# Kernel optimization log

Hardware: AMD Instinct MI355X
Metric: run time of the kernel (lower is better)

Reference implementation:

```python
import jax, jax.numpy as jnp
import numpy as np
from jax import lax

B, N, C, W, D = 128, 16384, 8, 10, 3   # batch, input_size, n_channels, out_window, poly_degree
L = N - W + 1                          # in-filter tap length
EPS = 1e-5


def setup_inputs() -> dict:
    key = jax.random.key(0)
    ks = jax.random.split(key, 8)
    x = jax.random.normal(ks[0], (B, N, C, 2), dtype=jnp.float32)
    # torch Linear-style scale ~ 1/sqrt(fan_in)
    w_in_real = jax.random.normal(ks[1], (C, L), dtype=jnp.float32) * (L ** -0.5)
    w_in_imag = jax.random.normal(ks[2], (C, L), dtype=jnp.float32) * (L ** -0.5)
    fan_coeff = 2 * (C - 1) * D
    w_coeff = jax.random.normal(ks[3], (C, 2, fan_coeff), dtype=jnp.float32) * (fan_coeff ** -0.5)
    w_out_real = jax.random.normal(ks[4], (C, W), dtype=jnp.float32) * (W ** -0.5)
    w_out_imag = jax.random.normal(ks[5], (C, W), dtype=jnp.float32) * (W ** -0.5)
    bn_gamma = jnp.ones((C,), dtype=jnp.float32)
    bn_beta = jnp.zeros((C,), dtype=jnp.float32)
    return {"x": x, "w_in_real": w_in_real, "w_in_imag": w_in_imag,
            "w_coeff": w_coeff, "w_out_real": w_out_real,
            "w_out_imag": w_out_imag, "bn_gamma": bn_gamma, "bn_beta": bn_beta}


# complement index map: row c lists all channels != c
_IDX = np.array([[j for j in range(C) if j != c] for c in range(C)])  # (C, C-1)


def _grouped_fir(sig, w):
    # sig: (B, N, C); per-channel length-L correlation -> (B, W, C)
    out = lax.conv_general_dilated(
        jnp.transpose(sig, (0, 2, 1)),      # (B, C, N)
        w[:, None, :],                      # (C, 1, L)
        window_strides=(1,), padding='VALID', feature_group_count=C)
    return jnp.transpose(out, (0, 2, 1))    # (B, W, C)


def reference(x, w_in_real, w_in_imag, w_coeff, w_out_real, w_out_imag, bn_gamma, bn_beta):
    fr = _grouped_fir(x[..., 0], w_in_real)   # (B, W, C)
    fi = _grouped_fir(x[..., 1], w_in_imag)   # (B, W, C)

    # polynomial expansion: pow_d = fr^d + fi^d, d = 1..D
    powd = jnp.stack([fr ** d + fi ** d for d in range(1, D + 1)], axis=-1)  # (B, W, C, D)
    poly_r = powd * fr[..., None]
    poly_i = powd * fi[..., None]

    # cross-channel coeff layers: input layout = [real(all j != c), imag(all j != c)]
    rg = poly_r[:, :, _IDX, :]                      # (B, W, C, C-1, D)
    ig = poly_i[:, :, _IDX, :]
    Wc = w_coeff.reshape(C, 2, 2, C - 1, D)         # (c, out, real/imag half, j, d)
    nonlin = (jnp.einsum('bwcjd,cpjd->bwcp', rg, Wc[:, :, 0]) +
              jnp.einsum('bwcjd,cpjd->bwcp', ig, Wc[:, :, 1]))  # (B, W, C, 2)

    out_r = jnp.einsum('bwc,cw->bc', nonlin[..., 0], w_out_real)
    out_i = jnp.einsum('bwc,cw->bc', nonlin[..., 1], w_out_imag)
    out = jnp.stack([out_r, out_i], axis=-1)        # (B, C, 2)

    # BatchNorm1d over (batch, last) per channel, training-mode batch stats
    mean = out.mean(axis=(0, 2), keepdims=True)
    var = out.var(axis=(0, 2), keepdims=True)
    return (out - mean) / jnp.sqrt(var + EPS) * bn_gamma[None, :, None] + bn_beta[None, :, None]
```

## Files before the change

kernel.cpp:

```cpp
#include <hip/hip_runtime.h>

#define BB 128
#define NN 16384
#define CC 8
#define WW 10
#define LL 16375
#define NT 512
#define NTILES (NN / NT)
#define BT 8
#define BTILES (BB / BT)
#define WSL (NT + 9)
#define SWSZ (WSL * 4 + 17)
#define BPB 2
#define ABLK (BB / BPB)

typedef float f4_t __attribute__((ext_vector_type(4)));

__global__ __launch_bounds__(512, 2) void k_fir(const float* __restrict__ x,
                                                const float* __restrict__ wr,
                                                const float* __restrict__ wi,
                                                float* __restrict__ fpart2) {
  __shared__ f4_t sw[SWSZ];
  int nt = blockIdx.x & (NTILES - 1);
  int bt = blockIdx.x >> 5;
  int tid = threadIdx.x;
  int ntile = nt * NT;
  int l0 = ntile - 9;

  {
    int c2s = tid & 3;
    int ca = 2 * c2s, cb = ca + 1;
    for (int j = tid >> 2; j < WSL; j += 128) {
      int l = l0 + j;
      f4_t v = (f4_t)0.f;
      if (l >= 0 && l < LL) {
        v[0] = wr[(size_t)ca * LL + l];
        v[1] = wi[(size_t)ca * LL + l];
        v[2] = wr[(size_t)cb * LL + l];
        v[3] = wi[(size_t)cb * LL + l];
      }
      sw[j * 4 + c2s + (j >> 5)] = v;
    }
  }
  __syncthreads();

  int wvb = tid >> 6;
  int b   = bt * BT + wvb;
  int c2  = tid & 3;
  int s   = (tid >> 2) & 15;
  int jbase = s * 32 + 9;

  const f4_t* __restrict__ xp = (const f4_t*)x + ((size_t)b * NN + ntile + s * 32) * 4 + c2;

#define TAP(q) sw[(jbase + (q)) * 4 + c2 + ((jbase + (q)) >> 5)]

  f4_t acc[WW];
#pragma unroll
  for (int w = 0; w < WW; ++w) acc[w] = (f4_t)0.f;

  f4_t wv[16];
#pragma unroll
  for (int k = 0; k < 9; ++k) wv[7 + k] = TAP(k - 9);

#pragma unroll
  for (int g = 0; g < 2; ++g) {
#pragma unroll
    for (int j = 0; j < 7; ++j) wv[j] = TAP(16 * g + j);
#pragma unroll
    for (int u = 0; u < 16; ++u) {
      f4_t xv = xp[(size_t)(16 * g + u) * 4];
#pragma unroll
      for (int w = 0; w < WW; ++w) {
        f4_t wt = wv[(u - w + 16) & 15];
        acc[w] += xv * wt;
      }
      if (u <= 8) wv[u + 7] = TAP(16 * g + u + 7);
    }
  }

#pragma unroll
  for (int w = 0; w < WW; ++w)
#pragma unroll
    for (int e = 0; e < 4; ++e) {
      acc[w][e] += __shfl_xor(acc[w][e], 4);
      acc[w][e] += __shfl_xor(acc[w][e], 8);
      acc[w][e] += __shfl_xor(acc[w][e], 16);
      acc[w][e] += __shfl_xor(acc[w][e], 32);
    }

  int lane = tid & 63;
  if (lane < 40) {
    int wsel = lane >> 2;
    f4_t myacc = (f4_t)0.f;
#pragma unroll
    for (int w = 0; w < WW; ++w)
      if (w == wsel) myacc = acc[w];
#pragma unroll
    for (int e = 0; e < 4; ++e)
      fpart2[((size_t)(wsel * 16 + c2 * 4 + e) * BB + b) * NTILES + nt] = myacc[e];
  }
}

__global__ __launch_bounds__(256) void k_nonlin(const float* __restrict__ fpart2,
                                                const float* __restrict__ wc,
                                                const float* __restrict__ wor,
                                                const float* __restrict__ woi,
                                                float* __restrict__ oraw,
                                                float* __restrict__ part) {
  __shared__ float sred[BPB][164];
  __shared__ float swc[672];
  __shared__ float swout[160];

  int tid = threadIdx.x;
  int blk = blockIdx.x;
  int b0 = blk * BPB;

  for (int i = tid; i < 672; i += 256) swc[i] = wc[i];
  if (tid < 80) swout[tid] = wor[tid];
  else if (tid < 160) swout[tid] = woi[tid - 80];

  for (int t = tid; t < 2 * 160; t += 256) {
    int r = t >> 1, bl = t & 1;
    const f4_t* fp = (const f4_t*)(fpart2 + ((size_t)r * BB + b0 + bl) * NTILES);
    f4_t s4 = (f4_t)0.f;
#pragma unroll
    for (int k = 0; k < NTILES / 4; ++k) s4 += fp[k];
    sred[bl][r] = s4[0] + s4[1] + s4[2] + s4[3];
  }
  __syncthreads();

  if (tid < 32) {
    int bl = tid >> 4;
    int c  = (tid >> 1) & 7;
    int p  = tid & 1;

    float wreg[8][2][3];
#pragma unroll
    for (int j = 0; j < 8; ++j) {
      int jj = j - (j > c ? 1 : 0);
      if (j == c) jj = 0;
#pragma unroll
      for (int ri = 0; ri < 2; ++ri)
#pragma unroll
        for (int d = 0; d < 3; ++d) {
          float v = swc[(c * 2 + p) * 42 + ri * 21 + jj * 3 + d];
          wreg[j][ri][d] = (j == c) ? 0.f : v;
        }
    }

    float o = 0.f;
    const float* wop = swout + p * 80 + c * 10;
#pragma unroll
    for (int w = 0; w < WW; ++w) {
      float4 f0 = *(const float4*)&sred[bl][w * 16];
      float4 f1 = *(const float4*)&sred[bl][w * 16 + 4];
      float4 f2 = *(const float4*)&sred[bl][w * 16 + 8];
      float4 f3 = *(const float4*)&sred[bl][w * 16 + 12];
      float fv[16] = {f0.x, f0.y, f0.z, f0.w, f1.x, f1.y, f1.z, f1.w,
                      f2.x, f2.y, f2.z, f2.w, f3.x, f3.y, f3.z, f3.w};
      float nl0 = 0.f, nl1 = 0.f, nl2 = 0.f;
#pragma unroll
      for (int j = 0; j < 8; ++j) {
        float r  = fv[2 * j];
        float im = fv[2 * j + 1];
        float r2 = r * r, i2 = im * im;
        float pw0 = r + im;
        float pw1 = r2 + i2;
        float pw2 = r2 * r + i2 * im;
        nl0 += (pw0 * r) * wreg[j][0][0] + (pw0 * im) * wreg[j][1][0];
        nl1 += (pw1 * r) * wreg[j][0][1] + (pw1 * im) * wreg[j][1][1];
        nl2 += (pw2 * r) * wreg[j][0][2] + (pw2 * im) * wreg[j][1][2];
      }
      o += (nl0 + nl1 + nl2) * wop[w];
    }

    oraw[((size_t)(b0 + bl) * CC + c) * 2 + p] = o;

    float s = o, q = o * o;
    s += __shfl_xor(s, 1);  q += __shfl_xor(q, 1);
    s += __shfl_xor(s, 16); q += __shfl_xor(q, 16);
    if ((tid & 17) == 0) {
      part[blk * 16 + c * 2 + 0] = s;
      part[blk * 16 + c * 2 + 1] = q;
    }
  }
}

__global__ __launch_bounds__(256) void k_bn(const float* __restrict__ oraw,
                                            const float* __restrict__ part,
                                            const float* __restrict__ gamma,
                                            const float* __restrict__ beta,
                                            float* __restrict__ out) {
  __shared__ float mv[8], iv[8], bv[8];
  int tid = threadIdx.x;
  if (tid < 16) {
    int cc = tid >> 1, qq = tid & 1;
    float s = 0.f;
#pragma unroll
    for (int k = 0; k < ABLK; ++k) s += part[k * 16 + cc * 2 + qq];
    float other = __shfl_xor(s, 1);
    if (qq == 0) {
      float mean = s * (1.0f / 256.0f);
      float var  = other * (1.0f / 256.0f) - mean * mean;
      mv[cc] = mean;
      iv[cc] = gamma[cc] * rsqrtf(var + 1e-5f);
      bv[cc] = beta[cc];
    }
  }
  __syncthreads();
  for (int i = tid; i < BB * CC * 2; i += 256) {
    int c = (i >> 1) & 7;
    out[i] = (oraw[i] - mv[c]) * iv[c] + bv[c];
  }
}

extern "C" void kernel_launch(void* const* d_in, const int* in_sizes, int n_in,
                              void* d_out, int out_size, void* d_ws, size_t ws_size,
                              hipStream_t stream) {
  const float* x   = (const float*)d_in[0];
  const float* wr  = (const float*)d_in[1];
  const float* wi  = (const float*)d_in[2];
  const float* wc  = (const float*)d_in[3];
  const float* wor = (const float*)d_in[4];
  const float* woi = (const float*)d_in[5];
  const float* gm  = (const float*)d_in[6];
  const float* bt  = (const float*)d_in[7];
  float* out = (float*)d_out;

  float* ws     = (float*)d_ws;
  float* fpart2 = ws;
  float* oraw   = fpart2 + (size_t)160 * BB * NTILES;
  float* part   = oraw + BB * CC * 2;

  k_fir<<<dim3(BTILES * NTILES), dim3(512), 0, stream>>>(x, wr, wi, fpart2);
  k_nonlin<<<dim3(ABLK), dim3(256), 0, stream>>>(fpart2, wc, wor, woi, oraw, part);
  k_bn<<<dim3(1), dim3(256), 0, stream>>>(oraw, part, gm, bt, out);
}
```

Baseline: 48.81 us.

## Remap FIR threads so each wave covers four batches sharing filter taps

Shrinks the FIR block to 256 threads covering 4 batches by 512 positions, with lanes arranged so a wave's 16-lane groups handle different batches at the same positions and so read the same LDS taps. The padded LDS layout is dropped, which removes per-tap index arithmetic. The cross-lane reduction shrinks to two shuffle steps, and the final sum over the four waves goes through shared memory. This trades fewer shuffles and broadcast LDS reads for an extra barrier and an LDS reduction stage, and the grid doubles in block count.

After: 48.37 us. About the same (-0.9%).

```diff
diff --git a/kernel.cpp b/kernel.cpp
--- a/kernel.cpp
+++ b/kernel.cpp
@@ -7,20 +7,22 @@
 #define LL 16375
 #define NT 512
 #define NTILES (NN / NT)
-#define BT 8
+#define BT 4
 #define BTILES (BB / BT)
 #define WSL (NT + 9)
-#define SWSZ (WSL * 4 + 17)
+#define SWSZ (WSL * 16 + 16)
 #define BPB 2
 #define ABLK (BB / BPB)
 
 typedef float f4_t __attribute__((ext_vector_type(4)));
 
-__global__ __launch_bounds__(512, 2) void k_fir(const float* __restrict__ x,
-                                                const float* __restrict__ wr,
-                                                const float* __restrict__ wi,
-                                                float* __restrict__ fpart2) {
-  __shared__ f4_t sw[SWSZ];
+__global__ __launch_bounds__(256) void k_fir(const float* __restrict__ x,
+                                             const float* __restrict__ wr,
+                                             const float* __restrict__ wi,
+                                             float* __restrict__ fpart2) {
+  __shared__ float smem[SWSZ];
+  f4_t* sw = (f4_t*)smem;
+
   int nt = blockIdx.x & (NTILES - 1);
   int bt = blockIdx.x >> 5;
   int tid = threadIdx.x;
@@ -28,9 +30,9 @@
   int l0 = ntile - 9;
 
   {
-    int c2s = tid & 3;
-    int ca = 2 * c2s, cb = ca + 1;
-    for (int j = tid >> 2; j < WSL; j += 128) {
+    int c2s = tid >> 6;
+    int ca = 2 * c2s, cb = 2 * c2s + 1;
+    for (int j = tid & 63; j < WSL; j += 64) {
       int l = l0 + j;
       f4_t v = (f4_t)0.f;
       if (l >= 0 && l < LL) {
@@ -39,20 +41,19 @@
         v[2] = wr[(size_t)cb * LL + l];
         v[3] = wi[(size_t)cb * LL + l];
       }
-      sw[j * 4 + c2s + (j >> 5)] = v;
-    }
-  }
-  __syncthreads();
-
-  int wvb = tid >> 6;
-  int b   = bt * BT + wvb;
-  int c2  = tid & 3;
-  int s   = (tid >> 2) & 15;
-  int jbase = s * 32 + 9;
-
-  const f4_t* __restrict__ xp = (const f4_t*)x + ((size_t)b * NN + ntile + s * 32) * 4 + c2;
-
-#define TAP(q) sw[(jbase + (q)) * 4 + c2 + ((jbase + (q)) >> 5)]
+      sw[j * 4 + c2s] = v;
+    }
+  }
+  __syncthreads();
+
+  int c2   = tid & 3;
+  int bsub = (tid >> 2) & 3;
+  int nh   = tid >> 4;
+  int b    = bt * BT + bsub;
+  int n0   = ntile + nh * 32;
+
+  const f4_t* __restrict__ xp = ((const f4_t*)x) + ((size_t)b * NN + n0) * 4 + c2;
+  const f4_t* swp = sw + (nh * 32 + 9) * 4 + c2;
 
   f4_t acc[WW];
 #pragma unroll
@@ -60,12 +61,12 @@
 
   f4_t wv[16];
 #pragma unroll
-  for (int k = 0; k < 9; ++k) wv[7 + k] = TAP(k - 9);
+  for (int k = 0; k < 9; ++k) wv[7 + k] = swp[4 * (k - 9)];
 
 #pragma unroll
   for (int g = 0; g < 2; ++g) {
 #pragma unroll
-    for (int j = 0; j < 7; ++j) wv[j] = TAP(16 * g + j);
+    for (int j = 0; j < 7; ++j) wv[j] = swp[4 * (16 * g + j)];
 #pragma unroll
     for (int u = 0; u < 16; ++u) {
       f4_t xv = xp[(size_t)(16 * g + u) * 4];
@@ -74,7 +75,7 @@
         f4_t wt = wv[(u - w + 16) & 15];
         acc[w] += xv * wt;
       }
-      if (u <= 8) wv[u + 7] = TAP(16 * g + u + 7);
+      if (u <= 8) wv[u + 7] = swp[4 * (16 * g + u + 7)];
     }
   }
 
@@ -82,22 +83,30 @@
   for (int w = 0; w < WW; ++w)
 #pragma unroll
     for (int e = 0; e < 4; ++e) {
-      acc[w][e] += __shfl_xor(acc[w][e], 4);
-      acc[w][e] += __shfl_xor(acc[w][e], 8);
       acc[w][e] += __shfl_xor(acc[w][e], 16);
       acc[w][e] += __shfl_xor(acc[w][e], 32);
     }
 
-  int lane = tid & 63;
-  if (lane < 40) {
-    int wsel = lane >> 2;
-    f4_t myacc = (f4_t)0.f;
+  __syncthreads();
+  int wave = tid >> 6, lane = tid & 63;
+  if (lane < 16) {
 #pragma unroll
     for (int w = 0; w < WW; ++w)
-      if (w == wsel) myacc = acc[w];
-#pragma unroll
-    for (int e = 0; e < 4; ++e)
-      fpart2[((size_t)(wsel * 16 + c2 * 4 + e) * BB + b) * NTILES + nt] = myacc[e];
+      *(f4_t*)&smem[(wave * 16 + lane) * 40 + w * 4] = acc[w];
+  }
+  __syncthreads();
+  for (int t = tid; t < BT * 160; t += 256) {
+    int bs = t / 160;
+    int r  = t - bs * 160;
+    int w  = r >> 4;
+    int cc = (r >> 1) & 7;
+    int ri = r & 1;
+    int ln = (cc >> 1) + 4 * bs;
+    int e  = (cc & 1) * 2 + ri;
+    float s = 0.f;
+#pragma unroll
+    for (int wv_ = 0; wv_ < 4; ++wv_) s += smem[(wv_ * 16 + ln) * 40 + w * 4 + e];
+    fpart2[((size_t)r * BB + (bt * BT + bs)) * NTILES + nt] = s;
   }
 }
 
@@ -232,7 +241,7 @@
   float* oraw   = fpart2 + (size_t)160 * BB * NTILES;
   float* part   = oraw + BB * CC * 2;
 
-  k_fir<<<dim3(BTILES * NTILES), dim3(512), 0, stream>>>(x, wr, wi, fpart2);
+  k_fir<<<dim3(BTILES * NTILES), dim3(256), 0, stream>>>(x, wr, wi, fpart2);
   k_nonlin<<<dim3(ABLK), dim3(256), 0, stream>>>(fpart2, wc, wor, woi, oraw, part);
   k_bn<<<dim3(1), dim3(256), 0, stream>>>(oraw, part, gm, bt, out);
 }
```
